# Kernel optimization log

Measured on AMD Instinct MI355X. Metric: run time of the kernel, lower is better.

The kernel has to match this reference:

```python
import jax, jax.numpy as jnp
import numpy as np


def setup_inputs() -> dict:
    key = jax.random.key(0)
    k1, k2, k3 = jax.random.split(key, 3)
    B, L, D = 8, 4096, 320
    CB_DIM, N_BOOKS = 16, 8192
    input_values = jax.random.normal(k1, (B, L, D), dtype=jnp.float32)
    # mask all ones -> static masked-select shape N = B*L
    mask_time_indices = jnp.ones((B, L), dtype=jnp.int32)
    # xavier_uniform for Linear(D -> CB_DIM, bias=False): limit = sqrt(6/(fan_in+fan_out))
    limit = float(np.sqrt(6.0 / (D + CB_DIM)))
    proj_weight = jax.random.uniform(k2, (CB_DIM, D), dtype=jnp.float32, minval=-limit, maxval=limit)
    code_book = jax.random.normal(k3, (N_BOOKS, CB_DIM), dtype=jnp.float32)
    return {"input_values": input_values, "mask_time_indices": mask_time_indices,
            "proj_weight": proj_weight, "code_book": code_book}


def reference(input_values, mask_time_indices, proj_weight, code_book):
    # input_values: [B, L, D]; mask is all-ones so masked select == flatten (static shape N=B*L)
    B, L, D = input_values.shape
    flat = input_values.reshape(B * L, D)  # [N, D]
    targets = flat @ proj_weight.T  # [N, cb_dim]  (random projection, no bias)
    # argmin over Euclidean norm == argmin over squared distance (monotone),
    # expanded form avoids the [N, n_books, cb_dim] broadcast intermediate.
    t2 = jnp.sum(targets * targets, axis=-1, keepdims=True)        # [N, 1]
    c2 = jnp.sum(code_book * code_book, axis=-1)                   # [n_books]
    d2 = t2 - 2.0 * (targets @ code_book.T) + c2                   # [N, n_books]
    labels = jnp.argmin(d2, axis=-1)                               # [N]
    return labels
```

## Files before the change

kernel.cpp:

```cpp
#include <hip/hip_runtime.h>

#define N_ROWS 32768
#define D_IN 320
#define CB 16
#define N_BOOKS 8192

typedef __attribute__((ext_vector_type(8))) short bf16x8;
typedef __attribute__((ext_vector_type(4))) float f32x4;
#define MFMA __builtin_amdgcn_mfma_f32_16x16x32_bf16
#define AS1 __attribute__((address_space(1)))
#define AS3 __attribute__((address_space(3)))

__device__ __forceinline__ unsigned short bf16rn(float f) {
  unsigned u = __float_as_uint(f);
  u += 0x7fffu + ((u >> 16) & 1u);
  return (unsigned short)(u >> 16);
}
__device__ __forceinline__ float bf16tof(unsigned short h) {
  return __uint_as_float(((unsigned)h) << 16);
}
__device__ __forceinline__ void gload_lds16(const short* g, short* l) {
  __builtin_amdgcn_global_load_lds((const AS1 unsigned int*)g, (AS3 unsigned int*)l, 16, 0, 0);
}

__global__ __launch_bounds__(256) void prep_kernel(const float* __restrict__ cbk,
                                                   short* __restrict__ bfrag,
                                                   float* __restrict__ nh_g) {
  const int j = blockIdx.x * 256 + threadIdx.x;
  const float4* src = (const float4*)(cbk + (size_t)j * CB);
  float4 a = src[0], b = src[1], c = src[2], d = src[3];
  float ce[16] = {a.x, a.y, a.z, a.w, b.x, b.y, b.z, b.w,
                  c.x, c.y, c.z, c.w, d.x, d.y, d.z, d.w};
  short c1[16], c2[16], c3[16];
  double s = 0.0;
#pragma unroll
  for (int i = 0; i < 16; i++) {
    s += (double)ce[i] * (double)ce[i];
    unsigned short x1 = bf16rn(ce[i]);
    float r1 = ce[i] - bf16tof(x1);
    unsigned short x2 = bf16rn(r1);
    float r2 = r1 - bf16tof(x2);
    unsigned short x3 = bf16rn(r2);
    c1[i] = (short)x1; c2[i] = (short)x2; c3[i] = (short)x3;
  }
  nh_g[j] = (float)(-0.5 * s);
  bf16x8 lo1, hi1, lo2, hi2, lo3, hi3;
#pragma unroll
  for (int i = 0; i < 8; i++) {
    lo1[i] = c1[i]; hi1[i] = c1[i + 8];
    lo2[i] = c2[i]; hi2[i] = c2[i + 8];
    lo3[i] = c3[i]; hi3[i] = c3[i + 8];
  }
  const int bt = j >> 4, n = j & 15;
  short* base = bfrag + (size_t)bt * 1536;
  *(bf16x8*)(base + 0 * 512 + (0 * 16 + n) * 8) = lo1;
  *(bf16x8*)(base + 0 * 512 + (1 * 16 + n) * 8) = hi1;
  *(bf16x8*)(base + 0 * 512 + (2 * 16 + n) * 8) = lo1;
  *(bf16x8*)(base + 0 * 512 + (3 * 16 + n) * 8) = hi1;
  *(bf16x8*)(base + 1 * 512 + (0 * 16 + n) * 8) = lo2;
  *(bf16x8*)(base + 1 * 512 + (1 * 16 + n) * 8) = hi2;
  *(bf16x8*)(base + 1 * 512 + (2 * 16 + n) * 8) = lo2;
  *(bf16x8*)(base + 1 * 512 + (3 * 16 + n) * 8) = hi2;
  *(bf16x8*)(base + 2 * 512 + (0 * 16 + n) * 8) = lo3;
  *(bf16x8*)(base + 2 * 512 + (1 * 16 + n) * 8) = hi3;
  *(bf16x8*)(base + 2 * 512 + (2 * 16 + n) * 8) = lo1;
  *(bf16x8*)(base + 2 * 512 + (3 * 16 + n) * 8) = hi1;
}

__global__ __launch_bounds__(256, 2) void proj_kernel(const float* __restrict__ x,
                                                      const float* __restrict__ w,
                                                      short* __restrict__ tsplit) {
  __shared__ __align__(16) short wfrag[3][10][64][8];
  __shared__ __align__(16) float xs[2][64 * 36];
  const int tid = threadIdx.x;
  const int lane = tid & 63;
  const int wv = tid >> 6;

  for (int i = tid; i < D_IN * CB; i += 256) {
    int d = i >> 4, o = i & 15;
    float f = w[o * D_IN + d];
    unsigned short h1 = bf16rn(f);
    float r1 = f - bf16tof(h1);
    unsigned short h2 = bf16rn(r1);
    float r2 = r1 - bf16tof(h2);
    unsigned short h3 = bf16rn(r2);
    int c = d >> 5, qq = (d >> 3) & 3, pos = d & 7;
    int ln = qq * 16 + o;
    wfrag[0][c][ln][pos] = (short)h1;
    wfrag[1][c][ln][pos] = (short)h2;
    wfrag[2][c][ln][pos] = (short)h3;
  }

  const float* xblk = x + (size_t)blockIdx.x * 64 * D_IN;
  {
    int row = tid >> 2, k0 = (tid & 3) * 8;
    float4 v0 = *(const float4*)(xblk + row * D_IN + k0);
    float4 v1 = *(const float4*)(xblk + row * D_IN + k0 + 4);
    *(float4*)&xs[0][row * 36 + k0] = v0;
    *(float4*)&xs[0][row * 36 + k0 + 4] = v1;
  }
  __syncthreads();

  const int m = lane & 15, q = lane >> 4;
  double dacc[4] = {0.0, 0.0, 0.0, 0.0};
  for (int c = 0; c < 10; c++) {
    const int buf = c & 1;
    if (c < 9) {
      int row = tid >> 2, k0 = (tid & 3) * 8;
      float4 v0 = *(const float4*)(xblk + row * D_IN + (c + 1) * 32 + k0);
      float4 v1 = *(const float4*)(xblk + row * D_IN + (c + 1) * 32 + k0 + 4);
      *(float4*)&xs[buf ^ 1][row * 36 + k0] = v0;
      *(float4*)&xs[buf ^ 1][row * 36 + k0 + 4] = v1;
    }
    const float* xp = &xs[buf][(wv * 16 + m) * 36 + q * 8];
    float4 xa = *(const float4*)xp;
    float4 xb = *(const float4*)(xp + 4);
    float xe[8] = {xa.x, xa.y, xa.z, xa.w, xb.x, xb.y, xb.z, xb.w};
    bf16x8 a1, a2, a3;
#pragma unroll
    for (int j = 0; j < 8; j++) {
      unsigned short h1 = bf16rn(xe[j]);
      float r1 = xe[j] - bf16tof(h1);
      unsigned short h2 = bf16rn(r1);
      float r2 = r1 - bf16tof(h2);
      unsigned short h3 = bf16rn(r2);
      a1[j] = (short)h1; a2[j] = (short)h2; a3[j] = (short)h3;
    }
    bf16x8 b1 = *(const bf16x8*)wfrag[0][c][lane];
    bf16x8 b2 = *(const bf16x8*)wfrag[1][c][lane];
    bf16x8 b3 = *(const bf16x8*)wfrag[2][c][lane];
    f32x4 g = {0.f, 0.f, 0.f, 0.f};
    g = MFMA(a1, b1, g, 0, 0, 0);
#pragma unroll
    for (int r = 0; r < 4; r++) dacc[r] += (double)g[r];
    g = (f32x4){0.f, 0.f, 0.f, 0.f};
    g = MFMA(a2, b1, g, 0, 0, 0);
    g = MFMA(a1, b2, g, 0, 0, 0);
#pragma unroll
    for (int r = 0; r < 4; r++) dacc[r] += (double)g[r];
    g = (f32x4){0.f, 0.f, 0.f, 0.f};
    g = MFMA(a3, b1, g, 0, 0, 0);
    g = MFMA(a1, b3, g, 0, 0, 0);
    g = MFMA(a2, b2, g, 0, 0, 0);
#pragma unroll
    for (int r = 0; r < 4; r++) dacc[r] += (double)g[r];
    __syncthreads();
  }

  float* tl = (float*)xs;
#pragma unroll
  for (int r = 0; r < 4; r++) tl[(wv * 16 + q * 4 + r) * 17 + m] = (float)dacc[r];
  __syncthreads();
  {
    int row_l = tid >> 2, p = tid & 3;
    short h1[4], h2[4], h3[4];
#pragma unroll
    for (int i = 0; i < 4; i++) {
      float f = tl[row_l * 17 + p * 4 + i];
      unsigned short a = bf16rn(f);
      float r1 = f - bf16tof(a);
      unsigned short b = bf16rn(r1);
      float r2 = r1 - bf16tof(b);
      unsigned short cc = bf16rn(r2);
      h1[i] = (short)a; h2[i] = (short)b; h3[i] = (short)cc;
    }
    size_t base = (size_t)(blockIdx.x * 64 + row_l) * 48;
    *(short4*)(tsplit + base + p * 4) = make_short4(h1[0], h1[1], h1[2], h1[3]);
    *(short4*)(tsplit + base + 16 + p * 4) = make_short4(h2[0], h2[1], h2[2], h2[3]);
    *(short4*)(tsplit + base + 32 + p * 4) = make_short4(h3[0], h3[1], h3[2], h3[3]);
  }
}

#define SC_H 4

__global__ __launch_bounds__(256, 2) void score_kernel(const short* __restrict__ tsplit,
                                                       const short* __restrict__ bfrag,
                                                       const float* __restrict__ nh_g,
                                                       float4* __restrict__ cand) {
  __shared__ __align__(16) short ldsb[2][12288];
  __shared__ float ldsnh[2048];
  const int tid = threadIdx.x;
  const int lane = tid & 63;
  const int wv = tid >> 6;
  const int m = lane & 15, q = lane >> 4;
  const int rb = blockIdx.x & 127;
  const int h = blockIdx.x >> 7;
  const int rowbase = rb * 256;

  bf16x8 A12[4], A13[4];
#pragma unroll
  for (int rt = 0; rt < 4; rt++) {
    int row = rowbase + wv * 64 + rt * 16 + m;
    const short* tp = tsplit + (size_t)row * 48;
    A12[rt] = *(const bf16x8*)(tp + q * 8);
    A13[rt] = *(const bf16x8*)(tp + q * 8 + ((q >= 2) ? 16 : 0));
  }
  for (int i = tid; i < 2048; i += 256) ldsnh[i] = nh_g[h * 2048 + i];

  const short* gq = bfrag + (size_t)h * 196608;
  {
    const short* g0 = gq + wv * 512 + lane * 8;
#pragma unroll
    for (int it = 0; it < 6; it++)
      gload_lds16(g0 + it * 2048, &ldsb[0][it * 2048 + wv * 512]);
  }

  float s1[4][4], s2[4][4];
  int i1[4][4];
#pragma unroll
  for (int rt = 0; rt < 4; rt++)
#pragma unroll
    for (int r = 0; r < 4; r++) { s1[rt][r] = -3.4e38f; s2[rt][r] = -3.4e38f; i1[rt][r] = 0; }

  __syncthreads();

  for (int sc = 0; sc < 16; sc++) {
    const int cur = sc & 1;
    if (sc < 15) {
      const short* gs = gq + (sc + 1) * 12288 + wv * 512 + lane * 8;
#pragma unroll
      for (int it = 0; it < 6; it++)
        gload_lds16(gs + it * 2048, &ldsb[cur ^ 1][it * 2048 + wv * 512]);
    }
#pragma unroll
    for (int bt = 0; bt < 8; bt++) {
      const short* bp = &ldsb[cur][bt * 1536];
      bf16x8 b1 = *(const bf16x8*)(bp + 0 * 512 + lane * 8);
      bf16x8 b2 = *(const bf16x8*)(bp + 1 * 512 + lane * 8);
      bf16x8 b3 = *(const bf16x8*)(bp + 2 * 512 + lane * 8);
      const int btg = sc * 8 + bt;
      float nh0 = ldsnh[btg * 16 + m];
      f32x4 ci = {nh0, nh0, nh0, nh0};
      const int colv = h * 2048 + btg * 16 + m;
#pragma unroll
      for (int rt = 0; rt < 4; rt++) {
        f32x4 acc = MFMA(A12[rt], b1, ci, 0, 0, 0);
        acc = MFMA(A12[rt], b2, acc, 0, 0, 0);
        acc = MFMA(A13[rt], b3, acc, 0, 0, 0);
#pragma unroll
        for (int r = 0; r < 4; r++) {
          float v = acc[r];
          float s1o = s1[rt][r];
          s2[rt][r] = __builtin_amdgcn_fmed3f(v, s1o, s2[rt][r]);
          s1[rt][r] = fmaxf(s1o, v);
          i1[rt][r] = (v > s1o) ? colv : i1[rt][r];
        }
      }
    }
    __syncthreads();
  }

#pragma unroll
  for (int rt = 0; rt < 4; rt++)
#pragma unroll
    for (int r = 0; r < 4; r++) {
      float a1v = s1[rt][r], a2v = s2[rt][r];
      int ai = i1[rt][r];
#pragma unroll
      for (int msk = 1; msk <= 8; msk <<= 1) {
        float o1 = __shfl_xor(a1v, msk);
        float o2 = __shfl_xor(a2v, msk);
        int oi = __shfl_xor(ai, msk);
        if (o1 > a1v) {
          a2v = fmaxf(a1v, o2); a1v = o1; ai = oi;
        } else {
          a2v = fmaxf(a2v, o1);
          if (o1 == a1v && oi < ai) ai = oi;
        }
      }
      if (m == 0) {
        int row = rowbase + wv * 64 + rt * 16 + q * 4 + r;
        cand[(size_t)h * N_ROWS + row] = make_float4(a1v, a2v, __int_as_float(ai), 0.f);
      }
    }
}

#define MARGIN_EPS 1.0e-4f

__global__ __launch_bounds__(256) void reduce_fb_kernel(const float4* __restrict__ cand,
                                                        const float* __restrict__ x,
                                                        const float* __restrict__ w,
                                                        const float* __restrict__ codebook,
                                                        int* __restrict__ out) {
  __shared__ int flagged[256];
  __shared__ double ps[16][17];
  __shared__ double tsh[16];
  __shared__ double rs[256];
  __shared__ int ri[256];
  const int tid = threadIdx.x;
  const int base = blockIdx.x * 256;
  {
    const int r = base + tid;
    float S1 = -3.4e38f, S2 = -3.4e38f;
    int I = 0;
#pragma unroll
    for (int h = 0; h < SC_H; h++) {
      float4 v = cand[(size_t)h * N_ROWS + r];
      if (v.x > S1) {
        S2 = fmaxf(S1, v.y); S1 = v.x; I = __float_as_int(v.z);
      } else {
        S2 = fmaxf(S2, v.x);
      }
    }
    out[r] = I;
    flagged[tid] = (S1 - S2 < MARGIN_EPS) ? 1 : 0;
  }
  __syncthreads();

  for (int rr = 0; rr < 256; rr++) {
    if (!flagged[rr]) continue;
    const int row = base + rr;
    {
      int o = tid & 15, c = tid >> 4;
      double p = 0.0;
      for (int k = 0; k < 20; k++) {
        int d = c * 20 + k;
        p = fma((double)x[(size_t)row * D_IN + d], (double)w[o * D_IN + d], p);
      }
      ps[c][o] = p;
    }
    __syncthreads();
    if (tid < 16) {
      double t = 0.0;
      for (int c = 0; c < 16; c++) t += ps[c][tid];
      tsh[tid] = t;
    }
    __syncthreads();
    double t[16];
#pragma unroll
    for (int i = 0; i < 16; i++) t[i] = tsh[i];
    double bs = -1.0e300;
    int bi = 0;
    for (int j = tid; j < N_BOOKS; j += 256) {
      const float* cp = codebook + (size_t)j * CB;
      double dot = 0.0, cc = 0.0;
#pragma unroll
      for (int i = 0; i < 16; i++) {
        double cv = (double)cp[i];
        dot = fma(t[i], cv, dot);
        cc = fma(cv, cv, cc);
      }
      double mv = dot - 0.5 * cc;
      if (mv > bs) { bs = mv; bi = j; }
    }
    rs[tid] = bs; ri[tid] = bi;
    __syncthreads();
    for (int s = 128; s > 0; s >>= 1) {
      if (tid < s) {
        double os = rs[tid + s]; int oi = ri[tid + s];
        if (os > rs[tid] || (os == rs[tid] && oi < ri[tid])) { rs[tid] = os; ri[tid] = oi; }
      }
      __syncthreads();
    }
    if (tid == 0) out[row] = ri[0];
    __syncthreads();
  }
}

extern "C" void kernel_launch(void* const* d_in, const int* in_sizes, int n_in,
                              void* d_out, int out_size, void* d_ws, size_t ws_size,
                              hipStream_t stream) {
  (void)in_sizes; (void)n_in; (void)out_size; (void)ws_size;
  const float* x = (const float*)d_in[0];
  const float* w = (const float*)d_in[2];
  const float* codebook = (const float*)d_in[3];

  char* ws = (char*)d_ws;
  short* tsplit = (short*)(ws);
  short* bfrag = (short*)(ws + (3 << 20));
  float* nh_g = (float*)(ws + 4718592);
  float4* cand = (float4*)(ws + (5 << 20));
  int* out = (int*)d_out;

  prep_kernel<<<N_BOOKS / 256, 256, 0, stream>>>(codebook, bfrag, nh_g);
  proj_kernel<<<N_ROWS / 64, 256, 0, stream>>>(x, w, tsplit);
  score_kernel<<<128 * SC_H, 256, 0, stream>>>(tsplit, bfrag, nh_g, cand);
  reduce_fb_kernel<<<N_ROWS / 256, 256, 0, stream>>>(cand, x, w, codebook, out);
}
```

Measured before the change: 202.3 us.

## Fuse prep into proj kernel, compact codebook fragments, split scoring across 8 chunks

Merges the codebook-prep and projection kernels into one launch, with the first 32 blocks doing codebook prep. The B-fragment layout drops its duplicated halves and lanes pick the right slice, which halves codebook global and LDS traffic. The score kernel now splits the codebook into 8 chunks instead of 4, giving twice as many blocks, half the LDS per block and a 4-block occupancy hint. Candidates are written as separate arrays rather than float4, and the weight load loop is reordered for coalesced reads. In exchange, the reduce step merges more partial results per row, and the higher occupancy hint may constrain register allocation.

Result: slower. 208.6 us (+3.1%).

```diff
diff --git a/kernel.cpp b/kernel.cpp
--- a/kernel.cpp
+++ b/kernel.cpp
@@ -23,75 +23,77 @@
   __builtin_amdgcn_global_load_lds((const AS1 unsigned int*)g, (AS3 unsigned int*)l, 16, 0, 0);
 }
 
-__global__ __launch_bounds__(256) void prep_kernel(const float* __restrict__ cbk,
-                                                   short* __restrict__ bfrag,
-                                                   float* __restrict__ nh_g) {
-  const int j = blockIdx.x * 256 + threadIdx.x;
-  const float4* src = (const float4*)(cbk + (size_t)j * CB);
-  float4 a = src[0], b = src[1], c = src[2], d = src[3];
-  float ce[16] = {a.x, a.y, a.z, a.w, b.x, b.y, b.z, b.w,
-                  c.x, c.y, c.z, c.w, d.x, d.y, d.z, d.w};
-  short c1[16], c2[16], c3[16];
-  double s = 0.0;
-#pragma unroll
-  for (int i = 0; i < 16; i++) {
-    s += (double)ce[i] * (double)ce[i];
-    unsigned short x1 = bf16rn(ce[i]);
-    float r1 = ce[i] - bf16tof(x1);
-    unsigned short x2 = bf16rn(r1);
-    float r2 = r1 - bf16tof(x2);
-    unsigned short x3 = bf16rn(r2);
-    c1[i] = (short)x1; c2[i] = (short)x2; c3[i] = (short)x3;
-  }
-  nh_g[j] = (float)(-0.5 * s);
-  bf16x8 lo1, hi1, lo2, hi2, lo3, hi3;
-#pragma unroll
-  for (int i = 0; i < 8; i++) {
-    lo1[i] = c1[i]; hi1[i] = c1[i + 8];
-    lo2[i] = c2[i]; hi2[i] = c2[i + 8];
-    lo3[i] = c3[i]; hi3[i] = c3[i + 8];
-  }
-  const int bt = j >> 4, n = j & 15;
-  short* base = bfrag + (size_t)bt * 1536;
-  *(bf16x8*)(base + 0 * 512 + (0 * 16 + n) * 8) = lo1;
-  *(bf16x8*)(base + 0 * 512 + (1 * 16 + n) * 8) = hi1;
-  *(bf16x8*)(base + 0 * 512 + (2 * 16 + n) * 8) = lo1;
-  *(bf16x8*)(base + 0 * 512 + (3 * 16 + n) * 8) = hi1;
-  *(bf16x8*)(base + 1 * 512 + (0 * 16 + n) * 8) = lo2;
-  *(bf16x8*)(base + 1 * 512 + (1 * 16 + n) * 8) = hi2;
-  *(bf16x8*)(base + 1 * 512 + (2 * 16 + n) * 8) = lo2;
-  *(bf16x8*)(base + 1 * 512 + (3 * 16 + n) * 8) = hi2;
-  *(bf16x8*)(base + 2 * 512 + (0 * 16 + n) * 8) = lo3;
-  *(bf16x8*)(base + 2 * 512 + (1 * 16 + n) * 8) = hi3;
-  *(bf16x8*)(base + 2 * 512 + (2 * 16 + n) * 8) = lo1;
-  *(bf16x8*)(base + 2 * 512 + (3 * 16 + n) * 8) = hi1;
-}
-
-__global__ __launch_bounds__(256, 2) void proj_kernel(const float* __restrict__ x,
-                                                      const float* __restrict__ w,
-                                                      short* __restrict__ tsplit) {
+__global__ __launch_bounds__(256, 2) void prep_proj_kernel(const float* __restrict__ cbk,
+                                                           const float* __restrict__ x,
+                                                           const float* __restrict__ w,
+                                                           short* __restrict__ bfrag,
+                                                           float* __restrict__ nh_g,
+                                                           short* __restrict__ tsplit) {
   __shared__ __align__(16) short wfrag[3][10][64][8];
   __shared__ __align__(16) float xs[2][64 * 36];
   const int tid = threadIdx.x;
+
+  if (blockIdx.x < 32) {
+    const int j = blockIdx.x * 256 + tid;
+    const float4* src = (const float4*)(cbk + (size_t)j * CB);
+    float4 a = src[0], b = src[1], c = src[2], d = src[3];
+    float ce[16] = {a.x, a.y, a.z, a.w, b.x, b.y, b.z, b.w,
+                    c.x, c.y, c.z, c.w, d.x, d.y, d.z, d.w};
+    short c1[16], c2[16], c3[16];
+    double s = 0.0;
+#pragma unroll
+    for (int i = 0; i < 16; i++) {
+      s += (double)ce[i] * (double)ce[i];
+      unsigned short x1 = bf16rn(ce[i]);
+      float r1 = ce[i] - bf16tof(x1);
+      unsigned short x2 = bf16rn(r1);
+      float r2 = r1 - bf16tof(x2);
+      unsigned short x3 = bf16rn(r2);
+      c1[i] = (short)x1; c2[i] = (short)x2; c3[i] = (short)x3;
+    }
+    nh_g[j] = (float)(-0.5 * s);
+    bf16x8 lo1, hi1, lo2, hi2, lo3, hi3;
+#pragma unroll
+    for (int i = 0; i < 8; i++) {
+      lo1[i] = c1[i]; hi1[i] = c1[i + 8];
+      lo2[i] = c2[i]; hi2[i] = c2[i + 8];
+      lo3[i] = c3[i]; hi3[i] = c3[i + 8];
+    }
+    short* base = bfrag + (size_t)(j >> 4) * 768;
+    const int n = j & 15;
+    *(bf16x8*)(base + 0 + n * 8) = lo1;
+    *(bf16x8*)(base + 128 + n * 8) = hi1;
+    *(bf16x8*)(base + 256 + n * 8) = lo2;
+    *(bf16x8*)(base + 384 + n * 8) = hi2;
+    *(bf16x8*)(base + 512 + n * 8) = lo3;
+    *(bf16x8*)(base + 640 + n * 8) = hi3;
+    return;
+  }
+
+  const int bid = blockIdx.x - 32;
   const int lane = tid & 63;
   const int wv = tid >> 6;
 
-  for (int i = tid; i < D_IN * CB; i += 256) {
-    int d = i >> 4, o = i & 15;
-    float f = w[o * D_IN + d];
-    unsigned short h1 = bf16rn(f);
-    float r1 = f - bf16tof(h1);
-    unsigned short h2 = bf16rn(r1);
-    float r2 = r1 - bf16tof(h2);
-    unsigned short h3 = bf16rn(r2);
-    int c = d >> 5, qq = (d >> 3) & 3, pos = d & 7;
-    int ln = qq * 16 + o;
-    wfrag[0][c][ln][pos] = (short)h1;
-    wfrag[1][c][ln][pos] = (short)h2;
-    wfrag[2][c][ln][pos] = (short)h3;
-  }
-
-  const float* xblk = x + (size_t)blockIdx.x * 64 * D_IN;
+  for (int o = 0; o < CB; o++) {
+    for (int dbase = 0; dbase < D_IN; dbase += 256) {
+      int d = dbase + tid;
+      if (d < D_IN) {
+        float f = w[o * D_IN + d];
+        unsigned short h1 = bf16rn(f);
+        float r1 = f - bf16tof(h1);
+        unsigned short h2 = bf16rn(r1);
+        float r2 = r1 - bf16tof(h2);
+        unsigned short h3 = bf16rn(r2);
+        int c = d >> 5, qq = (d >> 3) & 3, pos = d & 7;
+        int ln = qq * 16 + o;
+        wfrag[0][c][ln][pos] = (short)h1;
+        wfrag[1][c][ln][pos] = (short)h2;
+        wfrag[2][c][ln][pos] = (short)h3;
+      }
+    }
+  }
+
+  const float* xblk = x + (size_t)bid * 64 * D_IN;
   {
     int row = tid >> 2, k0 = (tid & 3) * 8;
     float4 v0 = *(const float4*)(xblk + row * D_IN + k0);
@@ -164,21 +166,23 @@
       unsigned short cc = bf16rn(r2);
       h1[i] = (short)a; h2[i] = (short)b; h3[i] = (short)cc;
     }
-    size_t base = (size_t)(blockIdx.x * 64 + row_l) * 48;
+    size_t base = (size_t)(bid * 64 + row_l) * 48;
     *(short4*)(tsplit + base + p * 4) = make_short4(h1[0], h1[1], h1[2], h1[3]);
     *(short4*)(tsplit + base + 16 + p * 4) = make_short4(h2[0], h2[1], h2[2], h2[3]);
     *(short4*)(tsplit + base + 32 + p * 4) = make_short4(h3[0], h3[1], h3[2], h3[3]);
   }
 }
 
-#define SC_H 4
-
-__global__ __launch_bounds__(256, 2) void score_kernel(const short* __restrict__ tsplit,
+#define SC_H 8
+
+__global__ __launch_bounds__(256, 4) void score_kernel(const short* __restrict__ tsplit,
                                                        const short* __restrict__ bfrag,
                                                        const float* __restrict__ nh_g,
-                                                       float4* __restrict__ cand) {
-  __shared__ __align__(16) short ldsb[2][12288];
-  __shared__ float ldsnh[2048];
+                                                       float* __restrict__ cs1,
+                                                       float* __restrict__ cs2,
+                                                       int* __restrict__ cidx) {
+  __shared__ __align__(16) short ldsb[2][6144];
+  __shared__ float ldsnh[1024];
   const int tid = threadIdx.x;
   const int lane = tid & 63;
   const int wv = tid >> 6;
@@ -195,14 +199,14 @@
     A12[rt] = *(const bf16x8*)(tp + q * 8);
     A13[rt] = *(const bf16x8*)(tp + q * 8 + ((q >= 2) ? 16 : 0));
   }
-  for (int i = tid; i < 2048; i += 256) ldsnh[i] = nh_g[h * 2048 + i];
-
-  const short* gq = bfrag + (size_t)h * 196608;
+  for (int i = tid; i < 1024; i += 256) ldsnh[i] = nh_g[h * 1024 + i];
+
+  const short* gq = bfrag + (size_t)h * 49152;
   {
-    const short* g0 = gq + wv * 512 + lane * 8;
-#pragma unroll
-    for (int it = 0; it < 6; it++)
-      gload_lds16(g0 + it * 2048, &ldsb[0][it * 2048 + wv * 512]);
+    const short* g0 = gq + wv * 1536 + lane * 8;
+#pragma unroll
+    for (int it = 0; it < 3; it++)
+      gload_lds16(g0 + it * 512, &ldsb[0][wv * 1536 + it * 512]);
   }
 
   float s1[4][4], s2[4][4];
@@ -214,24 +218,25 @@
 
   __syncthreads();
 
-  for (int sc = 0; sc < 16; sc++) {
+  for (int sc = 0; sc < 8; sc++) {
     const int cur = sc & 1;
-    if (sc < 15) {
-      const short* gs = gq + (sc + 1) * 12288 + wv * 512 + lane * 8;
-#pragma unroll
-      for (int it = 0; it < 6; it++)
-        gload_lds16(gs + it * 2048, &ldsb[cur ^ 1][it * 2048 + wv * 512]);
-    }
-#pragma unroll
+    if (sc < 7) {
+      const short* gs = gq + (sc + 1) * 6144 + wv * 1536 + lane * 8;
+#pragma unroll
+      for (int it = 0; it < 3; it++)
+        gload_lds16(gs + it * 512, &ldsb[cur ^ 1][wv * 1536 + it * 512]);
+    }
+#pragma unroll 2
     for (int bt = 0; bt < 8; bt++) {
-      const short* bp = &ldsb[cur][bt * 1536];
-      bf16x8 b1 = *(const bf16x8*)(bp + 0 * 512 + lane * 8);
-      bf16x8 b2 = *(const bf16x8*)(bp + 1 * 512 + lane * 8);
-      bf16x8 b3 = *(const bf16x8*)(bp + 2 * 512 + lane * 8);
+      const short* bp = &ldsb[cur][bt * 768];
+      const int l31 = (lane & 31) * 8;
+      bf16x8 b1 = *(const bf16x8*)(bp + l31);
+      bf16x8 b2 = *(const bf16x8*)(bp + 256 + l31);
+      bf16x8 b3 = *(const bf16x8*)(bp + ((lane < 32) ? 512 : 0) + l31);
       const int btg = sc * 8 + bt;
       float nh0 = ldsnh[btg * 16 + m];
       f32x4 ci = {nh0, nh0, nh0, nh0};
-      const int colv = h * 2048 + btg * 16 + m;
+      const int colv = h * 1024 + btg * 16 + m;
 #pragma unroll
       for (int rt = 0; rt < 4; rt++) {
         f32x4 acc = MFMA(A12[rt], b1, ci, 0, 0, 0);
@@ -270,14 +275,17 @@
       }
       if (m == 0) {
         int row = rowbase + wv * 64 + rt * 16 + q * 4 + r;
-        cand[(size_t)h * N_ROWS + row] = make_float4(a1v, a2v, __int_as_float(ai), 0.f);
+        size_t idx = (size_t)h * N_ROWS + row;
+        cs1[idx] = a1v; cs2[idx] = a2v; cidx[idx] = ai;
       }
     }
 }
 
 #define MARGIN_EPS 1.0e-4f
 
-__global__ __launch_bounds__(256) void reduce_fb_kernel(const float4* __restrict__ cand,
+__global__ __launch_bounds__(256) void reduce_fb_kernel(const float* __restrict__ cs1,
+                                                        const float* __restrict__ cs2,
+                                                        const int* __restrict__ cidx,
                                                         const float* __restrict__ x,
                                                         const float* __restrict__ w,
                                                         const float* __restrict__ codebook,
@@ -295,11 +303,12 @@
     int I = 0;
 #pragma unroll
     for (int h = 0; h < SC_H; h++) {
-      float4 v = cand[(size_t)h * N_ROWS + r];
-      if (v.x > S1) {
-        S2 = fmaxf(S1, v.y); S1 = v.x; I = __float_as_int(v.z);
+      size_t idx = (size_t)h * N_ROWS + r;
+      float v1 = cs1[idx], v2 = cs2[idx];
+      if (v1 > S1) {
+        S2 = fmaxf(S1, v2); S1 = v1; I = cidx[idx];
       } else {
-        S2 = fmaxf(S2, v.x);
+        S2 = fmaxf(S2, v1);
       }
     }
     out[r] = I;
@@ -367,13 +376,14 @@
 
   char* ws = (char*)d_ws;
   short* tsplit = (short*)(ws);
-  short* bfrag = (short*)(ws + (3 << 20));
-  float* nh_g = (float*)(ws + 4718592);
-  float4* cand = (float4*)(ws + (5 << 20));
+  short* bfrag = (short*)(ws + 3145728);
+  float* nh_g = (float*)(ws + 3932160);
+  float* cs1 = (float*)(ws + (4 << 20));
+  float* cs2 = (float*)(ws + (5 << 20));
+  int* cidx = (int*)(ws + (6 << 20));
   int* out = (int*)d_out;
 
-  prep_kernel<<<N_BOOKS / 256, 256, 0, stream>>>(codebook, bfrag, nh_g);
-  proj_kernel<<<N_ROWS / 64, 256, 0, stream>>>(x, w, tsplit);
-  score_kernel<<<128 * SC_H, 256, 0, stream>>>(tsplit, bfrag, nh_g, cand);
-  reduce_fb_kernel<<<N_ROWS / 256, 256, 0, stream>>>(cand, x, w, codebook, out);
-}
+  prep_proj_kernel<<<32 + N_ROWS / 64, 256, 0, stream>>>(codebook, x, w, bfrag, nh_g, tsplit);
+  score_kernel<<<128 * SC_H, 256, 0, stream>>>(tsplit, bfrag, nh_g, cs1, cs2, cidx);
+  reduce_fb_kernel<<<N_ROWS / 256, 256, 0, stream>>>(cs1, cs2, cidx, x, w, codebook, out);
+}
```
